# Optimization experiments

Measured on AMD Instinct MI355X. Metric: run time of the kernel, lower is better.

The kernel has to match this reference:

```python
import jax, jax.numpy as jnp
import numpy as np

N, D, L, H = 4, 512, 2048, 8  # batch, feat_dim, seq_len, num_heads


def setup_inputs() -> dict:
    key = jax.random.key(0)
    k1, k2, k3, k4 = jax.random.split(key, 4)
    x = jax.random.normal(k1, (N, D, L), dtype=jnp.float32)
    w_qkv = jax.random.normal(k2, (3 * D, D, 1), dtype=jnp.float32) * 0.02   # 1x1 conv
    w_dw = jax.random.normal(k3, (3 * D, 1, 3), dtype=jnp.float32) * 0.02    # depthwise k=3
    w_proj = jax.random.normal(k4, (D, D, 1), dtype=jnp.float32) * 0.02      # 1x1 conv
    temperature = jnp.ones((1, H, 1, 1), dtype=jnp.float32)
    return {"x": x, "w_qkv": w_qkv, "w_dw": w_dw, "w_proj": w_proj, "temperature": temperature}


def _conv1x1(x, w):
    # x: (n, c_in, l), w: (c_out, c_in, 1)
    return jnp.einsum('oc,ncl->nol', w[:, :, 0], x)


def _l2norm(t, eps=1e-12):
    # matches F.normalize: t / max(||t||_2, eps) along last dim
    n = jnp.sqrt(jnp.sum(t * t, axis=-1, keepdims=True))
    return t / jnp.maximum(n, eps)


def reference(x, w_qkv, w_dw, w_proj, temperature):
    n, d, l = x.shape
    h = temperature.shape[1]
    dh = d // h

    qkv = _conv1x1(x, w_qkv)                               # (n, 3d, l)
    qkv = jax.lax.conv_general_dilated(
        qkv, w_dw, window_strides=(1,), padding=[(1, 1)],
        dimension_numbers=('NCH', 'OIH', 'NCH'),
        feature_group_count=3 * d)                          # depthwise conv, (n, 3d, l)

    q, k, v = jnp.split(qkv, 3, axis=1)                     # each (n, d, l)
    # (n, d, l) -> (n, h, dh, l) -> (n, h, l, dh)
    q = q.reshape(n, h, dh, l).transpose(0, 1, 3, 2)
    k = k.reshape(n, h, dh, l).transpose(0, 1, 3, 2)
    v = v.reshape(n, h, dh, l).transpose(0, 1, 3, 2)

    q = _l2norm(q)
    k = _l2norm(k)

    scores = jnp.einsum('nhqd,nhkd->nhqk', q, k) * temperature  # (n, h, l, l)
    attn = jax.nn.softmax(scores, axis=-1)
    out = jnp.einsum('nhqk,nhkd->nhqd', attn, v)                # (n, h, l, dh)
    out = out.transpose(0, 1, 3, 2).reshape(n, d, l)            # (n, d, l)
    return _conv1x1(out, w_proj)
```

## Files before the change

### kernel.cpp

```cpp
#include <hip/hip_runtime.h>
#include <hip/hip_bf16.h>
#include <cstdint>
#include <cstddef>

#define N_B 4
#define D_F 512
#define L_S 2048
#define H_N 8
#define DH  64
#define C3  (3*D_F)

typedef __attribute__((ext_vector_type(8)))  short short8;
typedef __attribute__((ext_vector_type(4)))  float f32x4;
typedef __attribute__((ext_vector_type(16))) float f32x16;

__device__ __forceinline__ unsigned int pk_bf16(float a, float b) {
    __hip_bfloat162 h = __float22bfloat162_rn(float2{a, b});
    union { __hip_bfloat162 h; unsigned int u; } cv;
    cv.h = h;
    return cv.u;
}
__device__ __forceinline__ unsigned short bf16_rn(float f) {
    union { float f; unsigned int u; } c; c.f = f;
    unsigned int r = c.u + 0x7FFF + ((c.u >> 16) & 1);
    return (unsigned short)(r >> 16);
}
__device__ __forceinline__ float bf16_f(unsigned short h) {
    union { unsigned int u; float f; } c; c.u = ((unsigned int)h) << 16;
    return c.f;
}

__device__ __forceinline__ void gll16(const unsigned short* g, unsigned short* l) {
    __builtin_amdgcn_global_load_lds(
        (const __attribute__((address_space(1))) unsigned int*)g,
        (__attribute__((address_space(3))) unsigned int*)l,
        16, 0, 0);
}

__global__ __launch_bounds__(256) void cvt_split(const float* __restrict__ src,
                                                 unsigned short* __restrict__ hi,
                                                 unsigned short* __restrict__ lo,
                                                 int n4) {
    int i = blockIdx.x * 256 + threadIdx.x;
    if (i >= n4) return;
    float4 v = ((const float4*)src)[i];
    ushort4 h, l;
    h.x = bf16_rn(v.x); l.x = bf16_rn(v.x - bf16_f(h.x));
    h.y = bf16_rn(v.y); l.y = bf16_rn(v.y - bf16_f(h.y));
    h.z = bf16_rn(v.z); l.z = bf16_rn(v.z - bf16_f(h.z));
    h.w = bf16_rn(v.w); l.w = bf16_rn(v.w - bf16_f(h.w));
    ((ushort4*)hi)[i] = h;
    ((ushort4*)lo)[i] = l;
}

__global__ __launch_bounds__(256) void cvt_xT(const float* __restrict__ x,
                                              unsigned short* __restrict__ xT,
                                              int C) {
    __shared__ float tile[64][65];
    const int tid = threadIdx.x;
    const int l0  = blockIdx.x * 64;
    const int c0  = blockIdx.y * 64;
    const int n   = blockIdx.z;

    const float* xn = x + (size_t)n * C * L_S;
#pragma unroll
    for (int r = 0; r < 16; ++r) {
        int c = r * 4 + (tid >> 6);
        int l = tid & 63;
        tile[c][l] = xn[(size_t)(c0 + c) * L_S + l0 + l];
    }
    __syncthreads();

    unsigned short* xn_t = xT + (size_t)n * L_S * C;
#pragma unroll
    for (int r = 0; r < 8; ++r) {
        int l  = r * 8 + (tid >> 5);
        int cp = tid & 31;
        unsigned int pk = pk_bf16(tile[cp * 2][l], tile[cp * 2 + 1][l]);
        *(unsigned int*)&xn_t[(size_t)(l0 + l) * C + c0 + cp * 2] = pk;
    }
}

template<int SPLIT, int OUT_BF16>
__global__ __launch_bounds__(256) void gemm_mfma2(const unsigned short* __restrict__ Whi,
                                                  const unsigned short* __restrict__ Wlo,
                                                  const unsigned short* __restrict__ XThi,
                                                  const unsigned short* __restrict__ XTlo,
                                                  void* __restrict__ Y,
                                                  int O, int C) {
    __shared__ unsigned short Wt[SPLIT ? 2 : 1][4][128 * 8];
    __shared__ unsigned short Xt[SPLIT ? 2 : 1][4][128 * 8];

    const int tid  = threadIdx.x;
    const int lane = tid & 63;
    const int w    = tid >> 6;
    const int g    = lane >> 4;
    const int c    = lane & 15;
    const int wr   = (w >> 1) * 64;
    const int wc   = (w & 1) * 64;
    const int l0   = blockIdx.x * 128;
    const int o0   = blockIdx.y * 128;
    const int n    = blockIdx.z;

    const unsigned short* XTn_hi = XThi + (size_t)n * L_S * C;
    const unsigned short* XTn_lo = SPLIT ? (XTlo + (size_t)n * L_S * C) : nullptr;

    const int rhalf = (w & 1) * 64;
    const int cpA   = w >> 1;
    const int cpB   = 2 + (w >> 1);
    const size_t wrowA = (size_t)(o0 + rhalf + lane) * C;
    const size_t xrowA = (size_t)(l0 + rhalf + lane) * C;

    f32x4 acc[4][4];
#pragma unroll
    for (int mt = 0; mt < 4; ++mt)
#pragma unroll
        for (int nt = 0; nt < 4; ++nt) acc[mt][nt] = (f32x4){0.f, 0.f, 0.f, 0.f};

    for (int c0 = 0; c0 < C; c0 += 32) {
        __syncthreads();
        gll16(Whi + wrowA + c0 + cpA * 8, &Wt[0][cpA][rhalf * 8]);
        gll16(Whi + wrowA + c0 + cpB * 8, &Wt[0][cpB][rhalf * 8]);
        gll16(XTn_hi + xrowA + c0 + cpA * 8, &Xt[0][cpA][rhalf * 8]);
        gll16(XTn_hi + xrowA + c0 + cpB * 8, &Xt[0][cpB][rhalf * 8]);
        if (SPLIT) {
            gll16(Wlo + wrowA + c0 + cpA * 8, &Wt[1][cpA][rhalf * 8]);
            gll16(Wlo + wrowA + c0 + cpB * 8, &Wt[1][cpB][rhalf * 8]);
            gll16(XTn_lo + xrowA + c0 + cpA * 8, &Xt[1][cpA][rhalf * 8]);
            gll16(XTn_lo + xrowA + c0 + cpB * 8, &Xt[1][cpB][rhalf * 8]);
        }
        __syncthreads();

        short8 a0[4], b0[4];
#pragma unroll
        for (int mt = 0; mt < 4; ++mt) a0[mt] = *(short8*)&Wt[0][g][(wr + mt * 16 + c) * 8];
#pragma unroll
        for (int nt = 0; nt < 4; ++nt) b0[nt] = *(short8*)&Xt[0][g][(wc + nt * 16 + c) * 8];

        if (SPLIT) {
            short8 a1[4], b1[4];
#pragma unroll
            for (int mt = 0; mt < 4; ++mt) a1[mt] = *(short8*)&Wt[1][g][(wr + mt * 16 + c) * 8];
#pragma unroll
            for (int nt = 0; nt < 4; ++nt) b1[nt] = *(short8*)&Xt[1][g][(wc + nt * 16 + c) * 8];
#pragma unroll
            for (int mt = 0; mt < 4; ++mt)
#pragma unroll
                for (int nt = 0; nt < 4; ++nt) {
                    acc[mt][nt] = __builtin_amdgcn_mfma_f32_16x16x32_bf16(a0[mt], b0[nt], acc[mt][nt], 0, 0, 0);
                    acc[mt][nt] = __builtin_amdgcn_mfma_f32_16x16x32_bf16(a0[mt], b1[nt], acc[mt][nt], 0, 0, 0);
                    acc[mt][nt] = __builtin_amdgcn_mfma_f32_16x16x32_bf16(a1[mt], b0[nt], acc[mt][nt], 0, 0, 0);
                }
        } else {
#pragma unroll
            for (int mt = 0; mt < 4; ++mt)
#pragma unroll
                for (int nt = 0; nt < 4; ++nt)
                    acc[mt][nt] = __builtin_amdgcn_mfma_f32_16x16x32_bf16(a0[mt], b0[nt], acc[mt][nt], 0, 0, 0);
        }
    }

#pragma unroll
    for (int mt = 0; mt < 4; ++mt) {
#pragma unroll
        for (int r = 0; r < 4; ++r) {
            int oo = o0 + wr + mt * 16 + g * 4 + r;
            size_t rowbase = ((size_t)n * O + oo) * L_S;
#pragma unroll
            for (int nt = 0; nt < 4; ++nt) {
                int ll = l0 + wc + nt * 16 + c;
                if (OUT_BF16)
                    ((unsigned short*)Y)[rowbase + ll] = bf16_rn(acc[mt][nt][r]);
                else
                    ((float*)Y)[rowbase + ll] = acc[mt][nt][r];
            }
        }
    }
}

__global__ __launch_bounds__(256) void fused_qk2(const unsigned short* __restrict__ qkv_bf,
                                                 const float* __restrict__ w_dw,
                                                 unsigned short* __restrict__ Qb,
                                                 unsigned short* __restrict__ Kb) {
    __shared__ unsigned short rows[64 * 264];
    __shared__ float wsm[192];
    const int tid = threadIdx.x;
    const int l0  = blockIdx.x * 256;
    const int gg  = blockIdx.y;
    const int n   = blockIdx.z;
    const int head = gg & 7;
    const int ch0  = (gg < 8) ? head * 64 : 512 + head * 64;

    if (tid < 192) wsm[tid] = w_dw[ch0 * 3 + tid];

    const unsigned short* base = qkv_bf + ((size_t)n * C3 + ch0) * L_S;
    for (int f = tid; f < 2048; f += 256) {
        int e = f >> 5, s = f & 31;
        *(uint4*)&rows[e * 264 + s * 8] = *(const uint4*)&base[(size_t)e * L_S + l0 + s * 8];
    }
    if (tid < 64) {
        rows[tid * 264 + 256] = (l0 > 0) ? base[(size_t)tid * L_S + l0 - 1] : (unsigned short)0;
    } else if (tid < 128) {
        int e = tid - 64;
        rows[e * 264 + 257] = (l0 + 256 < L_S) ? base[(size_t)e * L_S + l0 + 256] : (unsigned short)0;
    }
    __syncthreads();

    const int lL = tid;
    const int iL = (lL == 0)   ? 256 : lL - 1;
    const int iR = (lL == 255) ? 257 : lL + 1;
    float y[64];
    float s = 0.f;
#pragma unroll
    for (int e = 0; e < 64; ++e) {
        float a = bf16_f(rows[e * 264 + iL]);
        float b = bf16_f(rows[e * 264 + lL]);
        float d = bf16_f(rows[e * 264 + iR]);
        float v = wsm[e * 3 + 0] * a + wsm[e * 3 + 1] * b + wsm[e * 3 + 2] * d;
        y[e] = v;
        s += v * v;
    }
    float sc = 1.0f / fmaxf(sqrtf(s), 1e-12f);

    const int l = l0 + tid;
    unsigned short* dst = ((gg < 8) ? Qb : Kb) + (size_t)(n * H_N + head) * 8 * L_S * 8;
#pragma unroll
    for (int p = 0; p < 8; ++p) {
        uint4 pk = make_uint4(pk_bf16(y[8 * p + 0] * sc, y[8 * p + 1] * sc),
                              pk_bf16(y[8 * p + 2] * sc, y[8 * p + 3] * sc),
                              pk_bf16(y[8 * p + 4] * sc, y[8 * p + 5] * sc),
                              pk_bf16(y[8 * p + 6] * sc, y[8 * p + 7] * sc));
        *(uint4*)&dst[((size_t)p * L_S + l) * 8] = pk;
    }
}

__global__ __launch_bounds__(256) void fused_v2(const unsigned short* __restrict__ qkv_bf,
                                                const float* __restrict__ w_dw,
                                                unsigned short* __restrict__ Vb) {
    const int tid = threadIdx.x;
    const int e   = tid & 63;
    const int jp  = blockIdx.x * 4 + (tid >> 6);
    const int h   = blockIdx.y;
    const int n   = blockIdx.z;
    const int ch  = 1024 + h * 64 + e;
    const unsigned short* row = qkv_bf + ((size_t)n * C3 + ch) * L_S;
    const int k0 = jp * 8;

    uint4 mv = *(const uint4*)&row[k0];
    unsigned int lw = (jp > 0)   ? *(const unsigned int*)&row[k0 - 2] : 0u;
    unsigned int rw = (jp < 255) ? *(const unsigned int*)&row[k0 + 8] : 0u;

    float v[10];
    v[0] = bf16_f((unsigned short)(lw >> 16));
    v[1] = bf16_f((unsigned short)(mv.x & 0xFFFF));
    v[2] = bf16_f((unsigned short)(mv.x >> 16));
    v[3] = bf16_f((unsigned short)(mv.y & 0xFFFF));
    v[4] = bf16_f((unsigned short)(mv.y >> 16));
    v[5] = bf16_f((unsigned short)(mv.z & 0xFFFF));
    v[6] = bf16_f((unsigned short)(mv.z >> 16));
    v[7] = bf16_f((unsigned short)(mv.w & 0xFFFF));
    v[8] = bf16_f((unsigned short)(mv.w >> 16));
    v[9] = bf16_f((unsigned short)(rw & 0xFFFF));

    float w0 = w_dw[ch * 3 + 0], w1 = w_dw[ch * 3 + 1], w2 = w_dw[ch * 3 + 2];
    unsigned int o[4];
#pragma unroll
    for (int i = 0; i < 4; ++i) {
        float y0 = w0 * v[2 * i + 0] + w1 * v[2 * i + 1] + w2 * v[2 * i + 2];
        float y1 = w0 * v[2 * i + 1] + w1 * v[2 * i + 2] + w2 * v[2 * i + 3];
        o[i] = pk_bf16(y0, y1);
    }
    uint4 ov = make_uint4(o[0], o[1], o[2], o[3]);
    *(uint4*)&Vb[(((size_t)(n * H_N + h) * 256 + jp) * 512) + e * 8] = ov;
}

__global__ __launch_bounds__(256, 3) void attn8(const unsigned short* __restrict__ Qb,
                                                const unsigned short* __restrict__ Kb,
                                                const unsigned short* __restrict__ Vb,
                                                const float* __restrict__ temp,
                                                unsigned short* __restrict__ aoT_hi,
                                                unsigned short* __restrict__ aoT_lo) {
    __shared__ float Ot[128 * 64];
    __shared__ float sm[128];

    const int tid  = threadIdx.x;
    const int lane = tid & 63;
    const int w    = tid >> 6;
    const int c32  = lane & 31;
    const int h    = lane >> 5;
    const int q0   = blockIdx.x * 128;
    const int hd   = blockIdx.y;
    const int n    = blockIdx.z;

    const size_t hb = (size_t)(n * H_N + hd);
    const unsigned short* Qh = Qb + hb * 8 * L_S * 8;
    const unsigned short* Kh = Kb + hb * 8 * L_S * 8;
    const unsigned short* Vh = Vb + hb * 256 * 512;
    const float t    = temp[hd];
    const float negm = -fabsf(t);

    short8 qa[4];
#pragma unroll
    for (int es = 0; es < 4; ++es)
        qa[es] = *(const short8*)&Qh[((size_t)(es * 2 + h) * L_S + q0 + w * 32 + c32) * 8];

    f32x16 acc0, acc1;
#pragma unroll
    for (int i = 0; i < 16; ++i) { acc0[i] = 0.f; acc1[i] = 0.f; }
    float sumP = 0.f;

    for (int k0 = 0; k0 < L_S; k0 += 64) {
        short8 vb0[4], vb1[4];
#pragma unroll
        for (int ks = 0; ks < 4; ++ks) {
            const unsigned short* vrow = Vh + (size_t)((k0 >> 3) + ks * 2 + h) * 512;
            vb0[ks] = *(const short8*)&vrow[c32 * 8];
            vb1[ks] = *(const short8*)&vrow[(32 + c32) * 8];
        }

        f32x16 sf0, sf1;
#pragma unroll
        for (int i = 0; i < 16; ++i) { sf0[i] = 0.f; sf1[i] = 0.f; }
        short8 ka0[4], ka1[4];
#pragma unroll
        for (int es = 0; es < 4; ++es) {
            const unsigned short* krow = Kh + (size_t)(es * 2 + h) * L_S * 8;
            ka0[es] = *(const short8*)&krow[(k0 + c32) * 8];
            ka1[es] = *(const short8*)&krow[(k0 + 32 + c32) * 8];
        }
        __builtin_amdgcn_s_setprio(1);
#pragma unroll
        for (int es = 0; es < 4; ++es) {
            sf0 = __builtin_amdgcn_mfma_f32_32x32x16_bf16(ka0[es], qa[es], sf0, 0, 0, 0);
            sf1 = __builtin_amdgcn_mfma_f32_32x32x16_bf16(ka1[es], qa[es], sf1, 0, 0, 0);
        }
        __builtin_amdgcn_s_setprio(0);

        short8 pa[4];
        {
            unsigned int W_[16], R_[16];
#pragma unroll
            for (int G = 0; G < 4; ++G) {
                float p0 = __expf(fmaf(sf0[4*G+0], t, negm));
                float p1 = __expf(fmaf(sf0[4*G+1], t, negm));
                float p2 = __expf(fmaf(sf0[4*G+2], t, negm));
                float p3 = __expf(fmaf(sf0[4*G+3], t, negm));
                sumP += (p0 + p1) + (p2 + p3);
                W_[2*G]   = pk_bf16(p0, p1);
                W_[2*G+1] = pk_bf16(p2, p3);
                float u0 = __expf(fmaf(sf1[4*G+0], t, negm));
                float u1 = __expf(fmaf(sf1[4*G+1], t, negm));
                float u2 = __expf(fmaf(sf1[4*G+2], t, negm));
                float u3 = __expf(fmaf(sf1[4*G+3], t, negm));
                sumP += (u0 + u1) + (u2 + u3);
                W_[8+2*G]   = pk_bf16(u0, u1);
                W_[8+2*G+1] = pk_bf16(u2, u3);
            }
#pragma unroll
            for (int j = 0; j < 16; ++j) R_[j] = __shfl_xor(W_[j], 32);
#pragma unroll
            for (int ks = 0; ks < 4; ++ks) {
                const int bb = (ks >> 1) * 8;
                const int m4 = (ks & 1) * 4;
                unsigned int a0 = h ? R_[bb+m4+2] : W_[bb+m4+0];
                unsigned int a1 = h ? R_[bb+m4+3] : W_[bb+m4+1];
                unsigned int a2 = h ? W_[bb+m4+2] : R_[bb+m4+0];
                unsigned int a3 = h ? W_[bb+m4+3] : R_[bb+m4+1];
                uint4 pu = make_uint4(a0, a1, a2, a3);
                pa[ks] = *(short8*)&pu;
            }
        }

        __builtin_amdgcn_s_setprio(1);
#pragma unroll
        for (int ks = 0; ks < 4; ++ks) {
            acc0 = __builtin_amdgcn_mfma_f32_32x32x16_bf16(pa[ks], vb0[ks], acc0, 0, 0, 0);
            acc1 = __builtin_amdgcn_mfma_f32_32x32x16_bf16(pa[ks], vb1[ks], acc1, 0, 0, 0);
        }
        __builtin_amdgcn_s_setprio(0);
    }

    sumP += __shfl_xor(sumP, 32);
    sm[w * 32 + c32] = 1.0f / sumP;

    float inv[16];
#pragma unroll
    for (int r = 0; r < 16; ++r) {
        int ql = (r & 3) + 8 * (r >> 2) + 4 * h;
        inv[r] = sm[w * 32 + ql];
    }

#pragma unroll
    for (int r = 0; r < 16; ++r) {
        int ql = (r & 3) + 8 * (r >> 2) + 4 * h;
        int qg = w * 32 + ql;
        Ot[qg * 64 + (c32 ^ (qg & 31))]        = acc0[r] * inv[r];
        Ot[qg * 64 + ((32 + c32) ^ (qg & 31))] = acc1[r] * inv[r];
    }
    __syncthreads();

    for (int tt = tid; tt < 8192; tt += 256) {
        int qq = tt >> 6, e = tt & 63;
        float v = Ot[qq * 64 + (e ^ (qq & 31))];
        unsigned short hi_ = bf16_rn(v);
        unsigned short lo_ = bf16_rn(v - bf16_f(hi_));
        size_t off = ((size_t)n * L_S + q0 + qq) * D_F + hd * 64 + e;
        aoT_hi[off] = hi_;
        aoT_lo[off] = lo_;
    }
}

extern "C" void kernel_launch(void* const* d_in, const int* in_sizes, int n_in,
                              void* d_out, int out_size, void* d_ws, size_t ws_size,
                              hipStream_t stream) {
    const float* x      = (const float*)d_in[0];
    const float* w_qkv  = (const float*)d_in[1];
    const float* w_dw   = (const float*)d_in[2];
    const float* w_proj = (const float*)d_in[3];
    const float* temp   = (const float*)d_in[4];
    float* out = (float*)d_out;

    const size_t WQE = (size_t)C3 * D_F;
    const size_t WPE = (size_t)D_F * D_F;

    char* ws = (char*)d_ws;
    unsigned short* qkv_bf = (unsigned short*)ws;
    unsigned short* Qb     = (unsigned short*)(ws + 25165824);
    unsigned short* Kb     = (unsigned short*)(ws + 33554432);
    unsigned short* Vb     = (unsigned short*)(ws + 41943040);
    unsigned short* xT     = (unsigned short*)(ws + 50331648);
    unsigned short* aoT_lo = (unsigned short*)(ws + 58720256);
    unsigned short* wq_hi  = (unsigned short*)(ws + 67108864);
    unsigned short* wq_lo  = wq_hi + WQE;
    unsigned short* wp_hi  = (unsigned short*)(ws + 70254592);
    unsigned short* wp_lo  = wp_hi + WPE;
    unsigned short* aoT_hi = xT;

    cvt_xT<<<dim3(L_S / 64, D_F / 64, N_B), 256, 0, stream>>>(x, xT, D_F);
    cvt_split<<<dim3((WQE / 4 + 255) / 256), 256, 0, stream>>>(w_qkv, wq_hi, wq_lo, WQE / 4);
    cvt_split<<<dim3((WPE / 4 + 255) / 256), 256, 0, stream>>>(w_proj, wp_hi, wp_lo, WPE / 4);

    gemm_mfma2<0, 1><<<dim3(L_S / 128, C3 / 128, N_B), 256, 0, stream>>>(
        wq_hi, nullptr, xT, nullptr, qkv_bf, C3, D_F);

    fused_qk2<<<dim3(L_S / 256, 16, N_B), 256, 0, stream>>>(qkv_bf, w_dw, Qb, Kb);
    fused_v2<<<dim3(64, H_N, N_B), 256, 0, stream>>>(qkv_bf, w_dw, Vb);

    attn8<<<dim3(L_S / 128, H_N, N_B), 256, 0, stream>>>(Qb, Kb, Vb, temp, aoT_hi, aoT_lo);

    gemm_mfma2<1, 0><<<dim3(L_S / 128, D_F / 128, N_B), 256, 0, stream>>>(
        wp_hi, wp_lo, aoT_hi, aoT_lo, out, D_F, D_F);
}
```

Measured before the change: 154.2 us.

## Split attention key range across two wave groups per block and merge

The attention kernel now launches 512 threads per block: two groups of four waves each process alternating 64-key chunks for the same 128 queries, halving the serial key loop per wave. The second group writes its partial accumulators and row sums to shared memory, and the first group merges them and normalizes before the shared store-out. This raises the number of waves working on each query tile, since softmax uses a fixed max bound so partials combine additively. In exchange it adds an extra shared-memory round trip and barrier, and launch bounds change from 3 to 2 blocks per CU, which may limit registers.

```diff
diff --git a/kernel.cpp b/kernel.cpp
--- a/kernel.cpp
+++ b/kernel.cpp
@@ -274,18 +274,21 @@
     *(uint4*)&Vb[(((size_t)(n * H_N + h) * 256 + jp) * 512) + e * 8] = ov;
 }
 
-__global__ __launch_bounds__(256, 3) void attn8(const unsigned short* __restrict__ Qb,
+__global__ __launch_bounds__(512, 2) void attn9(const unsigned short* __restrict__ Qb,
                                                 const unsigned short* __restrict__ Kb,
                                                 const unsigned short* __restrict__ Vb,
                                                 const float* __restrict__ temp,
                                                 unsigned short* __restrict__ aoT_hi,
                                                 unsigned short* __restrict__ aoT_lo) {
     __shared__ float Ot[128 * 64];
-    __shared__ float sm[128];
+    __shared__ float smB[128];
+    __shared__ float smA[128];
 
     const int tid  = threadIdx.x;
     const int lane = tid & 63;
     const int w    = tid >> 6;
+    const int g2   = w >> 2;
+    const int wv   = w & 3;
     const int c32  = lane & 31;
     const int h    = lane >> 5;
     const int q0   = blockIdx.x * 128;
@@ -302,14 +305,16 @@
     short8 qa[4];
 #pragma unroll
     for (int es = 0; es < 4; ++es)
-        qa[es] = *(const short8*)&Qh[((size_t)(es * 2 + h) * L_S + q0 + w * 32 + c32) * 8];
+        qa[es] = *(const short8*)&Qh[((size_t)(es * 2 + h) * L_S + q0 + wv * 32 + c32) * 8];
 
     f32x16 acc0, acc1;
 #pragma unroll
     for (int i = 0; i < 16; ++i) { acc0[i] = 0.f; acc1[i] = 0.f; }
     float sumP = 0.f;
 
-    for (int k0 = 0; k0 < L_S; k0 += 64) {
+    for (int it = 0; it < 16; ++it) {
+        const int k0 = (it * 2 + g2) * 64;
+
         short8 vb0[4], vb1[4];
 #pragma unroll
         for (int ks = 0; ks < 4; ++ks) {
@@ -381,25 +386,42 @@
     }
 
     sumP += __shfl_xor(sumP, 32);
-    sm[w * 32 + c32] = 1.0f / sumP;
-
-    float inv[16];
-#pragma unroll
-    for (int r = 0; r < 16; ++r) {
-        int ql = (r & 3) + 8 * (r >> 2) + 4 * h;
-        inv[r] = sm[w * 32 + ql];
-    }
-
-#pragma unroll
-    for (int r = 0; r < 16; ++r) {
-        int ql = (r & 3) + 8 * (r >> 2) + 4 * h;
-        int qg = w * 32 + ql;
-        Ot[qg * 64 + (c32 ^ (qg & 31))]        = acc0[r] * inv[r];
-        Ot[qg * 64 + ((32 + c32) ^ (qg & 31))] = acc1[r] * inv[r];
+
+    if (g2 == 1) {
+        smB[wv * 32 + c32] = sumP;
+#pragma unroll
+        for (int r = 0; r < 16; ++r) {
+            int ql = (r & 3) + 8 * (r >> 2) + 4 * h;
+            int qg = wv * 32 + ql;
+            Ot[qg * 64 + c32]      = acc0[r];
+            Ot[qg * 64 + 32 + c32] = acc1[r];
+        }
+    } else {
+        smA[wv * 32 + c32] = sumP;
     }
     __syncthreads();
 
-    for (int tt = tid; tt < 8192; tt += 256) {
+    if (g2 == 0) {
+        float b0[16], b1[16], inv[16];
+#pragma unroll
+        for (int r = 0; r < 16; ++r) {
+            int ql = (r & 3) + 8 * (r >> 2) + 4 * h;
+            int qg = wv * 32 + ql;
+            b0[r] = Ot[qg * 64 + c32];
+            b1[r] = Ot[qg * 64 + 32 + c32];
+            inv[r] = 1.0f / (smA[qg] + smB[qg]);
+        }
+#pragma unroll
+        for (int r = 0; r < 16; ++r) {
+            int ql = (r & 3) + 8 * (r >> 2) + 4 * h;
+            int qg = wv * 32 + ql;
+            Ot[qg * 64 + (c32 ^ (qg & 31))]        = (acc0[r] + b0[r]) * inv[r];
+            Ot[qg * 64 + ((32 + c32) ^ (qg & 31))] = (acc1[r] + b1[r]) * inv[r];
+        }
+    }
+    __syncthreads();
+
+    for (int tt = tid; tt < 8192; tt += 512) {
         int qq = tt >> 6, e = tt & 63;
         float v = Ot[qq * 64 + (e ^ (qq & 31))];
         unsigned short hi_ = bf16_rn(v);
@@ -446,7 +468,7 @@
     fused_qk2<<<dim3(L_S / 256, 16, N_B), 256, 0, stream>>>(qkv_bf, w_dw, Qb, Kb);
     fused_v2<<<dim3(64, H_N, N_B), 256, 0, stream>>>(qkv_bf, w_dw, Vb);
 
-    attn8<<<dim3(L_S / 128, H_N, N_B), 256, 0, stream>>>(Qb, Kb, Vb, temp, aoT_hi, aoT_lo);
+    attn9<<<dim3(L_S / 128, H_N, N_B), 512, 0, stream>>>(Qb, Kb, Vb, temp, aoT_hi, aoT_lo);
 
     gemm_mfma2<1, 0><<<dim3(L_S / 128, D_F / 128, N_B), 256, 0, stream>>>(
         wp_hi, wp_lo, aoT_hi, aoT_lo, out, D_F, D_F);
```

Measured after the change: 157.4 us. 2.1% more time.
